# Optimization experiments

Measured on AMD Instinct MI355X. Metric: run time of the kernel, lower is better.

The kernel has to match this reference:

```python
import jax, jax.numpy as jnp
import numpy as np

THETA = 10000.0
B, S, D, H = 2, 2048, 1024, 16
DK = D // H


def setup_inputs() -> dict:
    key = jax.random.key(0)
    ks = jax.random.split(key, 5)
    std = float(np.sqrt(2.0 / (D + D)))  # get_std(in, out) with in==out==D
    x = jax.random.normal(ks[0], (B, S, D), dtype=jnp.float32)
    Wq = jax.random.normal(ks[1], (D, D), dtype=jnp.float32) * std
    Wk = jax.random.normal(ks[2], (D, D), dtype=jnp.float32) * std
    Wv = jax.random.normal(ks[3], (D, D), dtype=jnp.float32) * std
    Wo = jax.random.normal(ks[4], (D, D), dtype=jnp.float32) * std
    token_positions = jnp.broadcast_to(jnp.arange(S, dtype=jnp.int32), (B, S))
    return {"x": x, "Wq": Wq, "Wk": Wk, "Wv": Wv, "Wo": Wo,
            "token_positions": token_positions}


def _rope(x, pos):
    # x: [B, H, S, d] with interleaved pairs (even=x1, odd=x2); pos: [B, 1, S]
    d = x.shape[-1]
    inv_freq = THETA ** (-(jnp.arange(0, d, 2, dtype=jnp.float32) / d))  # [d/2]
    freqs = pos[..., None].astype(jnp.float32) * inv_freq               # [B,1,S,d/2]
    cos, sin = jnp.cos(freqs), jnp.sin(freqs)
    x1, x2 = x[..., 0::2], x[..., 1::2]
    r1 = cos * x1 - sin * x2
    r2 = sin * x1 + cos * x2
    return jnp.stack([r1, r2], axis=-1).reshape(x.shape)  # re-interleave


def reference(x, Wq, Wk, Wv, Wo, token_positions):
    # Linear is y = x @ W.T (torch weight layout [out, in])
    def split_heads(t):
        return t.reshape(B, S, H, DK).transpose(0, 2, 1, 3)  # [B,H,S,DK]

    Q = split_heads(x @ Wq.T)
    K = split_heads(x @ Wk.T)
    V = split_heads(x @ Wv.T)

    pos = token_positions[:, None, :]  # [B,1,S] broadcast over heads
    Q = _rope(Q, pos)
    K = _rope(K, pos)

    scale = 1.0 / jnp.sqrt(jnp.float32(DK))
    scores = jnp.einsum('bhqd,bhkd->bhqk', Q, K) * scale  # [B,H,S,S]
    causal = jnp.arange(S)[:, None] >= jnp.arange(S)[None, :]
    scores = jnp.where(causal, scores, -jnp.inf)
    weights = jax.nn.softmax(scores, axis=-1)
    attn = jnp.einsum('bhqk,bhkd->bhqd', weights, V)
    attn = attn.transpose(0, 2, 1, 3).reshape(B, S, D)
    return attn @ Wo.T
```

## Files before the change

kernel.cpp:

```cpp
#include <hip/hip_runtime.h>
#include <hip/hip_bf16.h>
#include <math.h>

#define B_ 2
#define S_ 2048
#define D_ 1024
#define H_ 16
#define DK_ 64

typedef __bf16 bf16_t;
typedef bf16_t bf16x8 __attribute__((ext_vector_type(8)));
typedef bf16_t bf16x4 __attribute__((ext_vector_type(4)));
typedef float f32x4 __attribute__((ext_vector_type(4)));

__device__ __forceinline__ void gload16(const void* g, void* lds_base_uniform) {
  __builtin_amdgcn_global_load_lds(
      (const __attribute__((address_space(1))) unsigned int*)g,
      (__attribute__((address_space(3))) unsigned int*)lds_base_uniform, 16, 0, 0);
}

__global__ __launch_bounds__(256) void cast_bf16_vec(const float* __restrict__ in,
                                                     bf16_t* __restrict__ out, int n4) {
  int i = blockIdx.x * 256 + threadIdx.x;
  if (i >= n4) return;
  float4 f = reinterpret_cast<const float4*>(in)[i];
  bf16x4 o;
  o[0] = (bf16_t)f.x; o[1] = (bf16_t)f.y; o[2] = (bf16_t)f.z; o[3] = (bf16_t)f.w;
  reinterpret_cast<bf16x4*>(out)[i] = o;
}

__global__ __launch_bounds__(256) void cast_weights(const float* __restrict__ Wq,
                                                    const float* __restrict__ Wk,
                                                    const float* __restrict__ Wv,
                                                    const float* __restrict__ Wo,
                                                    bf16_t* __restrict__ out) {
  int i = blockIdx.x * 256 + threadIdx.x;
  int r = i >> 18;
  const float* src = (r == 0) ? Wq : (r == 1) ? Wk : (r == 2) ? Wv : Wo;
  float4 f = reinterpret_cast<const float4*>(src)[i & 262143];
  bf16x4 o;
  o[0] = (bf16_t)f.x; o[1] = (bf16_t)f.y; o[2] = (bf16_t)f.z; o[3] = (bf16_t)f.w;
  reinterpret_cast<bf16x4*>(out)[i] = o;
}

template <bool OUT_F32>
__global__ __launch_bounds__(256) void gemm_bt(const bf16_t* __restrict__ A,
                                               const bf16_t* __restrict__ W,
                                               void* __restrict__ Cout,
                                               int Ndim, int Kdim) {
  __shared__ __attribute__((aligned(16))) bf16_t As[128][64];
  __shared__ __attribute__((aligned(16))) bf16_t Bs[128][64];
  const int bm = blockIdx.x * 128;
  const int bn = blockIdx.y * 128;
  const int tid = threadIdx.x;
  const int lane = tid & 63;
  const int w = tid >> 6;
  const int wr = w >> 1, wc = w & 1;
  const int srow_in_chunk = lane >> 3;
  const int scol = (lane & 7) << 3;

  f32x4 acc[4][4];
  for (int m = 0; m < 4; ++m)
    for (int n = 0; n < 4; ++n) acc[m][n] = (f32x4){0.f, 0.f, 0.f, 0.f};

  for (int k0 = 0; k0 < Kdim; k0 += 64) {
    __syncthreads();
#pragma unroll
    for (int it = 0; it < 4; ++it) {
      const int c = w * 4 + it;
      const int r = c * 8 + srow_in_chunk;
      gload16(&A[(size_t)(bm + r) * Kdim + k0 + scol], (char*)&As[0][0] + c * 1024);
      gload16(&W[(size_t)(bn + r) * Kdim + k0 + scol], (char*)&Bs[0][0] + c * 1024);
    }
    __syncthreads();
#pragma unroll
    for (int t = 0; t < 2; ++t) {
      const int kk = t * 32 + ((lane >> 4) << 3);
      bf16x8 af[4], bfr[4];
#pragma unroll
      for (int m = 0; m < 4; ++m)
        af[m] = *reinterpret_cast<const bf16x8*>(&As[wr * 64 + m * 16 + (lane & 15)][kk]);
#pragma unroll
      for (int n = 0; n < 4; ++n)
        bfr[n] = *reinterpret_cast<const bf16x8*>(&Bs[wc * 64 + n * 16 + (lane & 15)][kk]);
#pragma unroll
      for (int m = 0; m < 4; ++m)
#pragma unroll
        for (int n = 0; n < 4; ++n)
          acc[m][n] = __builtin_amdgcn_mfma_f32_16x16x32_bf16(af[m], bfr[n], acc[m][n], 0, 0, 0);
    }
  }

  const int rg = (lane >> 4) << 2, c0 = lane & 15;
#pragma unroll
  for (int m = 0; m < 4; ++m)
#pragma unroll
    for (int n = 0; n < 4; ++n) {
      int r = bm + wr * 64 + m * 16 + rg;
      int c = bn + wc * 64 + n * 16 + c0;
#pragma unroll
      for (int i = 0; i < 4; ++i) {
        if (OUT_F32)
          reinterpret_cast<float*>(Cout)[(size_t)(r + i) * Ndim + c] = acc[m][n][i];
        else
          reinterpret_cast<bf16_t*>(Cout)[(size_t)(r + i) * Ndim + c] = (bf16_t)acc[m][n][i];
      }
    }
}

__global__ __launch_bounds__(256) void gemm_qkv(const bf16_t* __restrict__ A,
                                                const bf16_t* __restrict__ W,
                                                const int* __restrict__ posids,
                                                bf16_t* __restrict__ Qr,
                                                bf16_t* __restrict__ Kr,
                                                bf16_t* __restrict__ Vt) {
  __shared__ __attribute__((aligned(16))) bf16_t SMEM[2][128][64];
  const int bm = blockIdx.x * 128;
  const int bn = blockIdx.y * 128;
  const int tid = threadIdx.x;
  const int lane = tid & 63;
  const int w = tid >> 6;
  const int wr = w >> 1, wc = w & 1;
  const int srow_in_chunk = lane >> 3;
  const int scol = (lane & 7) << 3;
  const int Kdim = 1024;

  f32x4 acc[4][4];
  for (int m = 0; m < 4; ++m)
    for (int n = 0; n < 4; ++n) acc[m][n] = (f32x4){0.f, 0.f, 0.f, 0.f};

  for (int k0 = 0; k0 < Kdim; k0 += 64) {
    __syncthreads();
#pragma unroll
    for (int it = 0; it < 4; ++it) {
      const int c = w * 4 + it;
      const int r = c * 8 + srow_in_chunk;
      gload16(&A[(size_t)(bm + r) * Kdim + k0 + scol], (char*)&SMEM[0][0][0] + c * 1024);
      gload16(&W[(size_t)(bn + r) * Kdim + k0 + scol], (char*)&SMEM[1][0][0] + c * 1024);
    }
    __syncthreads();
#pragma unroll
    for (int t = 0; t < 2; ++t) {
      const int kk = t * 32 + ((lane >> 4) << 3);
      bf16x8 af[4], bfr[4];
#pragma unroll
      for (int m = 0; m < 4; ++m)
        af[m] = *reinterpret_cast<const bf16x8*>(&SMEM[0][wr * 64 + m * 16 + (lane & 15)][kk]);
#pragma unroll
      for (int n = 0; n < 4; ++n)
        bfr[n] = *reinterpret_cast<const bf16x8*>(&SMEM[1][wc * 64 + n * 16 + (lane & 15)][kk]);
#pragma unroll
      for (int m = 0; m < 4; ++m)
#pragma unroll
        for (int n = 0; n < 4; ++n)
          acc[m][n] = __builtin_amdgcn_mfma_f32_16x16x32_bf16(af[m], bfr[n], acc[m][n], 0, 0, 0);
    }
  }

  const int region = bn >> 10;
  const int h0 = (bn & 1023) >> 6;
  const int b = bm >> 11;
  const int sblk = bm & 2047;
  char* Cs = (char*)&SMEM[0][0][0];
  const int rg = (lane >> 4) << 2, c0 = lane & 15;

  __syncthreads();

  if (region < 2) {
#pragma unroll
    for (int m = 0; m < 4; ++m)
#pragma unroll
      for (int n = 0; n < 4; ++n) {
        const int col = wc * 64 + n * 16 + c0;
#pragma unroll
        for (int i = 0; i < 4; ++i) {
          const int row = wr * 64 + m * 16 + rg + i;
          *(bf16_t*)(Cs + row * 256 + ((col * 2) ^ ((row & 15) << 4))) = (bf16_t)acc[m][n][i];
        }
      }
    __syncthreads();
    const int sl = tid >> 1;
    const int hh = tid & 1;
    const int s = sblk + sl;
    const int bh = b * 16 + h0 + hh;
    const int p = posids[b * 2048 + s];
    bf16_t* outp = (region == 0 ? Qr : Kr) + ((size_t)bh * 2048 + s) * 64;
    const float qscale = region == 0 ? 0.125f : 1.0f;
#pragma unroll
    for (int j = 0; j < 8; ++j) {
      const int slot = hh * 8 + j;
      bf16x8 v = *(const bf16x8*)(Cs + sl * 256 + ((slot ^ (sl & 15)) << 4));
      bf16x8 ov;
#pragma unroll
      for (int e = 0; e < 8; e += 2) {
        const int ii = j * 4 + (e >> 1);
        float sn, cs2;
        __sincosf((float)p * __expf(-(float)(2 * ii) * (9.210340371976184f / 64.0f)),
                  &sn, &cs2);
        const float x1 = (float)v[e], x2 = (float)v[e + 1];
        ov[e]     = (bf16_t)((cs2 * x1 - sn * x2) * qscale);
        ov[e + 1] = (bf16_t)((sn * x1 + cs2 * x2) * qscale);
      }
      *(bf16x8*)(&outp[j * 8]) = ov;
    }
  } else {
#pragma unroll
    for (int m = 0; m < 4; ++m)
#pragma unroll
      for (int n = 0; n < 4; ++n) {
        const int col = wc * 64 + n * 16 + c0;
        const int row0 = wr * 64 + m * 16 + rg;
        bf16x4 pk;
#pragma unroll
        for (int i = 0; i < 4; ++i) pk[i] = (bf16_t)acc[m][n][i];
        *(bf16x4*)(Cs + col * 256 + ((row0 * 2) ^ ((col & 15) << 4))) = pk;
      }
    __syncthreads();
    const int dloc = tid >> 1;
    const int sg2 = tid & 1;
    const int bh = b * 16 + h0 + (dloc >> 6);
    const int d = dloc & 63;
    bf16_t* outp = Vt + ((size_t)bh * 64 + d) * 2048 + sblk + sg2 * 64;
#pragma unroll
    for (int j = 0; j < 8; ++j) {
      bf16x8 v = *(const bf16x8*)(Cs + dloc * 256 + (((sg2 * 8 + j) ^ (dloc & 15)) << 4));
      *(bf16x8*)(&outp[j * 8]) = v;
    }
  }
}

__global__ __launch_bounds__(256) void attn_kernel(const bf16_t* __restrict__ Qr,
                                                   const bf16_t* __restrict__ Kr,
                                                   const bf16_t* __restrict__ Vt,
                                                   bf16_t* __restrict__ AO) {
  const int linear = blockIdx.x;
  const int bh = linear & 31;
  const int qt = 31 - (linear >> 5);
  const int b = bh >> 4, h = bh & 15;
  const bf16_t* Qp = Qr + (size_t)bh * S_ * 64;
  const char* Kbase = (const char*)(Kr + (size_t)bh * S_ * 64);
  const char* Vbase = (const char*)(Vt + (size_t)bh * 64 * S_);
  const int tid = threadIdx.x, lane = tid & 63, w = tid >> 6;
  const int qb = qt * 64;
  const int nt = qt + 1;

  __shared__ __attribute__((aligned(16))) bf16_t Ksm[2][64][64];
  __shared__ __attribute__((aligned(16))) bf16_t Vts[2][64][64];
  __shared__ __attribute__((aligned(16))) bf16_t Psm[4][16][64];

  const int srow = lane >> 3;
  const int sslot = lane & 7;

  bf16x8 qf[2];
  {
    int qrow = qb + w * 16 + (lane & 15);
#pragma unroll
    for (int t = 0; t < 2; ++t)
      qf[t] = *reinterpret_cast<const bf16x8*>(
          &Qp[(size_t)qrow * 64 + t * 32 + ((lane >> 4) << 3)]);
  }

  f32x4 o[4];
  for (int m = 0; m < 4; ++m) o[m] = (f32x4){0.f, 0.f, 0.f, 0.f};
  float mrow = -1e30f, lrow = 0.f;

#pragma unroll
  for (int it = 0; it < 2; ++it) {
    int c = 2 * w + it;
    int row = c * 8 + srow;
    gload16(Kbase + (size_t)row * 128 + ((sslot ^ (row & 7)) << 4),
            (char*)&Ksm[0][0][0] + c * 1024);
    gload16(Vbase + (size_t)row * (S_ * 2) + ((sslot ^ (row & 7)) << 4),
            (char*)&Vts[0][0][0] + c * 1024);
  }
  __syncthreads();

  int cur = 0;
#pragma unroll 1
  for (int kt = 0; kt < nt; ++kt) {
    if (kt + 1 < nt) {
#pragma unroll
      for (int it = 0; it < 2; ++it) {
        int c = 2 * w + it;
        int row = c * 8 + srow;
        gload16(Kbase + (size_t)(kt + 1) * 8192 + (size_t)row * 128 + ((sslot ^ (row & 7)) << 4),
                (char*)&Ksm[cur ^ 1][0][0] + c * 1024);
        gload16(Vbase + (size_t)row * (S_ * 2) + (size_t)(kt + 1) * 128 + ((sslot ^ (row & 7)) << 4),
                (char*)&Vts[cur ^ 1][0][0] + c * 1024);
      }
    }

    f32x4 sacc[4];
    for (int m = 0; m < 4; ++m) sacc[m] = (f32x4){0.f, 0.f, 0.f, 0.f};
    __builtin_amdgcn_s_setprio(1);
#pragma unroll
    for (int t = 0; t < 2; ++t) {
      const int slot0 = t * 4 + (lane >> 4);
#pragma unroll
      for (int m = 0; m < 4; ++m) {
        const int R = m * 16 + (lane & 15);
        bf16x8 kfr = *reinterpret_cast<const bf16x8*>(
            (const char*)&Ksm[cur][0][0] + R * 128 + ((slot0 ^ (R & 7)) << 4));
        sacc[m] = __builtin_amdgcn_mfma_f32_16x16x32_bf16(kfr, qf[t], sacc[m], 0, 0, 0);
      }
    }
    __builtin_amdgcn_s_setprio(0);

    const int qrow = qb + w * 16 + (lane & 15);
    const int g4 = (lane >> 4) << 2;
    if (kt * 64 + 63 > qb + w * 16) {
#pragma unroll
      for (int m = 0; m < 4; ++m) {
        const int kc0 = kt * 64 + m * 16 + g4;
#pragma unroll
        for (int r = 0; r < 4; ++r)
          if (kc0 + r > qrow) sacc[m][r] = -1e30f;
      }
    }

    float mx = sacc[0][0];
#pragma unroll
    for (int m = 0; m < 4; ++m)
#pragma unroll
      for (int r = 0; r < 4; ++r) mx = fmaxf(mx, sacc[m][r]);
    mx = fmaxf(mx, __shfl_xor(mx, 16, 64));
    mx = fmaxf(mx, __shfl_xor(mx, 32, 64));
    const float mnew = fmaxf(mrow, mx);
    const float alpha = __expf(mrow - mnew);
    mrow = mnew;

    float s = 0.f;
#pragma unroll
    for (int m = 0; m < 4; ++m)
#pragma unroll
      for (int r = 0; r < 4; ++r) {
        float p = __expf(sacc[m][r] - mnew);
        sacc[m][r] = p;
        s += p;
      }
    s += __shfl_xor(s, 16, 64);
    s += __shfl_xor(s, 32, 64);
    lrow = lrow * alpha + s;

#pragma unroll
    for (int m = 0; m < 4; ++m)
#pragma unroll
      for (int r = 0; r < 4; ++r) o[m][r] *= alpha;

    {
      const int q = lane & 15;
      char* pbase = (char*)&Psm[w][0][0] + q * 128;
      const int xm = (q & 7) << 4;
#pragma unroll
      for (int m = 0; m < 4; ++m) {
        bf16x4 pk;
#pragma unroll
        for (int r = 0; r < 4; ++r) pk[r] = (bf16_t)sacc[m][r];
        *reinterpret_cast<bf16x4*>(pbase + (((m << 5) | ((lane >> 4) << 3)) ^ xm)) = pk;
      }
    }

    __builtin_amdgcn_s_setprio(1);
#pragma unroll
    for (int t = 0; t < 2; ++t) {
      const int slot0 = t * 4 + (lane >> 4);
      bf16x8 pf = *reinterpret_cast<const bf16x8*>(
          (const char*)&Psm[w][0][0] + (lane & 15) * 128 +
          (((t << 6) | ((lane >> 4) << 4)) ^ ((lane & 7) << 4)));
#pragma unroll
      for (int m = 0; m < 4; ++m) {
        const int R = m * 16 + (lane & 15);
        bf16x8 vf = *reinterpret_cast<const bf16x8*>(
            (const char*)&Vts[cur][0][0] + R * 128 + ((slot0 ^ (R & 7)) << 4));
        o[m] = __builtin_amdgcn_mfma_f32_16x16x32_bf16(vf, pf, o[m], 0, 0, 0);
      }
    }
    __builtin_amdgcn_s_setprio(0);

    __syncthreads();
    cur ^= 1;
  }

  {
    const int q = lane & 15;
    const int g4e = (lane >> 4) << 2;
    const int srw = qb + w * 16 + q;
    const float inv = 1.0f / lrow;
#pragma unroll
    for (int m = 0; m < 4; ++m) {
      bf16x4 ov;
#pragma unroll
      for (int r = 0; r < 4; ++r) ov[r] = (bf16_t)(o[m][r] * inv);
      *reinterpret_cast<bf16x4*>(
          &AO[((size_t)(b * S_ + srw)) * 1024 + h * 64 + m * 16 + g4e]) = ov;
    }
  }
}

extern "C" void kernel_launch(void* const* d_in, const int* in_sizes, int n_in,
                              void* d_out, int out_size, void* d_ws, size_t ws_size,
                              hipStream_t stream) {
  const float* x  = (const float*)d_in[0];
  const float* Wq = (const float*)d_in[1];
  const float* Wk = (const float*)d_in[2];
  const float* Wv = (const float*)d_in[3];
  const float* Wo = (const float*)d_in[4];
  const int* tp   = (const int*)d_in[5];

  char* ws = (char*)d_ws;
  bf16_t* xb   = (bf16_t*)(ws);
  bf16_t* Wcat = (bf16_t*)(ws + 8388608);
  bf16_t* Wob  = (bf16_t*)(ws + 14680064);
  bf16_t* Qr   = (bf16_t*)(ws + 41943040);
  bf16_t* Kr   = (bf16_t*)(ws + 50331648);
  bf16_t* Vt   = (bf16_t*)(ws + 58720256);
  bf16_t* AO   = (bf16_t*)(ws + 67108864);

  cast_bf16_vec<<<dim3(4096), dim3(256), 0, stream>>>(x, xb, 1048576);
  cast_weights<<<dim3(4096), dim3(256), 0, stream>>>(Wq, Wk, Wv, Wo, Wcat);

  gemm_qkv<<<dim3(32, 24), dim3(256), 0, stream>>>(xb, Wcat, tp, Qr, Kr, Vt);
  attn_kernel<<<dim3(1024), dim3(256), 0, stream>>>(Qr, Kr, Vt, AO);
  gemm_bt<true><<<dim3(32, 8), dim3(256), 0, stream>>>(AO, Wob, d_out, 1024, 1024);

  (void)in_sizes; (void)n_in; (void)out_size; (void)ws_size;
}
```

Before: 133.7 us.

## Double attention query tile to 128 rows with 8 waves per block

```diff
diff --git a/kernel.cpp b/kernel.cpp
--- a/kernel.cpp
+++ b/kernel.cpp
@@ -229,31 +229,32 @@
   }
 }
 
-__global__ __launch_bounds__(256) void attn_kernel(const bf16_t* __restrict__ Qr,
+__global__ __launch_bounds__(512) void attn_kernel(const bf16_t* __restrict__ Qr,
                                                    const bf16_t* __restrict__ Kr,
                                                    const bf16_t* __restrict__ Vt,
                                                    bf16_t* __restrict__ AO) {
   const int linear = blockIdx.x;
   const int bh = linear & 31;
-  const int qt = 31 - (linear >> 5);
+  const int qt = 15 - (linear >> 5);
   const int b = bh >> 4, h = bh & 15;
   const bf16_t* Qp = Qr + (size_t)bh * S_ * 64;
   const char* Kbase = (const char*)(Kr + (size_t)bh * S_ * 64);
   const char* Vbase = (const char*)(Vt + (size_t)bh * 64 * S_);
   const int tid = threadIdx.x, lane = tid & 63, w = tid >> 6;
-  const int qb = qt * 64;
-  const int nt = qt + 1;
+  const int qb = qt * 128;
+  const int nt = 2 * qt + 2;
+  const int wr0 = qb + w * 16;
 
   __shared__ __attribute__((aligned(16))) bf16_t Ksm[2][64][64];
   __shared__ __attribute__((aligned(16))) bf16_t Vts[2][64][64];
-  __shared__ __attribute__((aligned(16))) bf16_t Psm[4][16][64];
+  __shared__ __attribute__((aligned(16))) bf16_t Psm[8][16][64];
 
   const int srow = lane >> 3;
   const int sslot = lane & 7;
 
   bf16x8 qf[2];
   {
-    int qrow = qb + w * 16 + (lane & 15);
+    int qrow = wr0 + (lane & 15);
 #pragma unroll
     for (int t = 0; t < 2; ++t)
       qf[t] = *reinterpret_cast<const bf16x8*>(
@@ -264,14 +265,12 @@
   for (int m = 0; m < 4; ++m) o[m] = (f32x4){0.f, 0.f, 0.f, 0.f};
   float mrow = -1e30f, lrow = 0.f;
 
-#pragma unroll
-  for (int it = 0; it < 2; ++it) {
-    int c = 2 * w + it;
-    int row = c * 8 + srow;
+  {
+    int row = w * 8 + srow;
     gload16(Kbase + (size_t)row * 128 + ((sslot ^ (row & 7)) << 4),
-            (char*)&Ksm[0][0][0] + c * 1024);
+            (char*)&Ksm[0][0][0] + w * 1024);
     gload16(Vbase + (size_t)row * (S_ * 2) + ((sslot ^ (row & 7)) << 4),
-            (char*)&Vts[0][0][0] + c * 1024);
+            (char*)&Vts[0][0][0] + w * 1024);
   }
   __syncthreads();
 
@@ -279,103 +278,101 @@
 #pragma unroll 1
   for (int kt = 0; kt < nt; ++kt) {
     if (kt + 1 < nt) {
-#pragma unroll
-      for (int it = 0; it < 2; ++it) {
-        int c = 2 * w + it;
-        int row = c * 8 + srow;
-        gload16(Kbase + (size_t)(kt + 1) * 8192 + (size_t)row * 128 + ((sslot ^ (row & 7)) << 4),
-                (char*)&Ksm[cur ^ 1][0][0] + c * 1024);
-        gload16(Vbase + (size_t)row * (S_ * 2) + (size_t)(kt + 1) * 128 + ((sslot ^ (row & 7)) << 4),
-                (char*)&Vts[cur ^ 1][0][0] + c * 1024);
-      }
-    }
-
-    f32x4 sacc[4];
-    for (int m = 0; m < 4; ++m) sacc[m] = (f32x4){0.f, 0.f, 0.f, 0.f};
-    __builtin_amdgcn_s_setprio(1);
-#pragma unroll
-    for (int t = 0; t < 2; ++t) {
-      const int slot0 = t * 4 + (lane >> 4);
-#pragma unroll
-      for (int m = 0; m < 4; ++m) {
-        const int R = m * 16 + (lane & 15);
-        bf16x8 kfr = *reinterpret_cast<const bf16x8*>(
-            (const char*)&Ksm[cur][0][0] + R * 128 + ((slot0 ^ (R & 7)) << 4));
-        sacc[m] = __builtin_amdgcn_mfma_f32_16x16x32_bf16(kfr, qf[t], sacc[m], 0, 0, 0);
-      }
-    }
-    __builtin_amdgcn_s_setprio(0);
-
-    const int qrow = qb + w * 16 + (lane & 15);
-    const int g4 = (lane >> 4) << 2;
-    if (kt * 64 + 63 > qb + w * 16) {
-#pragma unroll
-      for (int m = 0; m < 4; ++m) {
-        const int kc0 = kt * 64 + m * 16 + g4;
-#pragma unroll
-        for (int r = 0; r < 4; ++r)
-          if (kc0 + r > qrow) sacc[m][r] = -1e30f;
-      }
-    }
-
-    float mx = sacc[0][0];
-#pragma unroll
-    for (int m = 0; m < 4; ++m)
-#pragma unroll
-      for (int r = 0; r < 4; ++r) mx = fmaxf(mx, sacc[m][r]);
-    mx = fmaxf(mx, __shfl_xor(mx, 16, 64));
-    mx = fmaxf(mx, __shfl_xor(mx, 32, 64));
-    const float mnew = fmaxf(mrow, mx);
-    const float alpha = __expf(mrow - mnew);
-    mrow = mnew;
-
-    float s = 0.f;
-#pragma unroll
-    for (int m = 0; m < 4; ++m)
-#pragma unroll
-      for (int r = 0; r < 4; ++r) {
-        float p = __expf(sacc[m][r] - mnew);
-        sacc[m][r] = p;
-        s += p;
-      }
-    s += __shfl_xor(s, 16, 64);
-    s += __shfl_xor(s, 32, 64);
-    lrow = lrow * alpha + s;
-
-#pragma unroll
-    for (int m = 0; m < 4; ++m)
-#pragma unroll
-      for (int r = 0; r < 4; ++r) o[m][r] *= alpha;
-
-    {
-      const int q = lane & 15;
-      char* pbase = (char*)&Psm[w][0][0] + q * 128;
-      const int xm = (q & 7) << 4;
-#pragma unroll
-      for (int m = 0; m < 4; ++m) {
-        bf16x4 pk;
-#pragma unroll
-        for (int r = 0; r < 4; ++r) pk[r] = (bf16_t)sacc[m][r];
-        *reinterpret_cast<bf16x4*>(pbase + (((m << 5) | ((lane >> 4) << 3)) ^ xm)) = pk;
-      }
-    }
-
-    __builtin_amdgcn_s_setprio(1);
-#pragma unroll
-    for (int t = 0; t < 2; ++t) {
-      const int slot0 = t * 4 + (lane >> 4);
-      bf16x8 pf = *reinterpret_cast<const bf16x8*>(
-          (const char*)&Psm[w][0][0] + (lane & 15) * 128 +
-          (((t << 6) | ((lane >> 4) << 4)) ^ ((lane & 7) << 4)));
-#pragma unroll
-      for (int m = 0; m < 4; ++m) {
-        const int R = m * 16 + (lane & 15);
-        bf16x8 vf = *reinterpret_cast<const bf16x8*>(
-            (const char*)&Vts[cur][0][0] + R * 128 + ((slot0 ^ (R & 7)) << 4));
-        o[m] = __builtin_amdgcn_mfma_f32_16x16x32_bf16(vf, pf, o[m], 0, 0, 0);
-      }
-    }
-    __builtin_amdgcn_s_setprio(0);
+      int row = w * 8 + srow;
+      gload16(Kbase + (size_t)(kt + 1) * 8192 + (size_t)row * 128 + ((sslot ^ (row & 7)) << 4),
+              (char*)&Ksm[cur ^ 1][0][0] + w * 1024);
+      gload16(Vbase + (size_t)row * (S_ * 2) + (size_t)(kt + 1) * 128 + ((sslot ^ (row & 7)) << 4),
+              (char*)&Vts[cur ^ 1][0][0] + w * 1024);
+    }
+
+    if (kt * 64 <= wr0 + 15) {
+      f32x4 sacc[4];
+      for (int m = 0; m < 4; ++m) sacc[m] = (f32x4){0.f, 0.f, 0.f, 0.f};
+      __builtin_amdgcn_s_setprio(1);
+#pragma unroll
+      for (int t = 0; t < 2; ++t) {
+        const int slot0 = t * 4 + (lane >> 4);
+#pragma unroll
+        for (int m = 0; m < 4; ++m) {
+          const int R = m * 16 + (lane & 15);
+          bf16x8 kfr = *reinterpret_cast<const bf16x8*>(
+              (const char*)&Ksm[cur][0][0] + R * 128 + ((slot0 ^ (R & 7)) << 4));
+          sacc[m] = __builtin_amdgcn_mfma_f32_16x16x32_bf16(kfr, qf[t], sacc[m], 0, 0, 0);
+        }
+      }
+      __builtin_amdgcn_s_setprio(0);
+
+      const int qrow = wr0 + (lane & 15);
+      const int g4 = (lane >> 4) << 2;
+      if (kt * 64 + 63 > wr0) {
+#pragma unroll
+        for (int m = 0; m < 4; ++m) {
+          const int kc0 = kt * 64 + m * 16 + g4;
+#pragma unroll
+          for (int r = 0; r < 4; ++r)
+            if (kc0 + r > qrow) sacc[m][r] = -1e30f;
+        }
+      }
+
+      float mx = sacc[0][0];
+#pragma unroll
+      for (int m = 0; m < 4; ++m)
+#pragma unroll
+        for (int r = 0; r < 4; ++r) mx = fmaxf(mx, sacc[m][r]);
+      mx = fmaxf(mx, __shfl_xor(mx, 16, 64));
+      mx = fmaxf(mx, __shfl_xor(mx, 32, 64));
+      const float mnew = fmaxf(mrow, mx);
+      const float alpha = __expf(mrow - mnew);
+      mrow = mnew;
+
+      float s = 0.f;
+#pragma unroll
+      for (int m = 0; m < 4; ++m)
+#pragma unroll
+        for (int r = 0; r < 4; ++r) {
+          float p = __expf(sacc[m][r] - mnew);
+          sacc[m][r] = p;
+          s += p;
+        }
+      s += __shfl_xor(s, 16, 64);
+      s += __shfl_xor(s, 32, 64);
+      lrow = lrow * alpha + s;
+
+#pragma unroll
+      for (int m = 0; m < 4; ++m)
+#pragma unroll
+        for (int r = 0; r < 4; ++r) o[m][r] *= alpha;
+
+      {
+        const int q = lane & 15;
+        char* pbase = (char*)&Psm[w][0][0] + q * 128;
+        const int xm = (q & 7) << 4;
+#pragma unroll
+        for (int m = 0; m < 4; ++m) {
+          bf16x4 pk;
+#pragma unroll
+          for (int r = 0; r < 4; ++r) pk[r] = (bf16_t)sacc[m][r];
+          *reinterpret_cast<bf16x4*>(pbase + (((m << 5) | ((lane >> 4) << 3)) ^ xm)) = pk;
+        }
+      }
+
+      __builtin_amdgcn_s_setprio(1);
+#pragma unroll
+      for (int t = 0; t < 2; ++t) {
+        const int slot0 = t * 4 + (lane >> 4);
+        bf16x8 pf = *reinterpret_cast<const bf16x8*>(
+            (const char*)&Psm[w][0][0] + (lane & 15) * 128 +
+            (((t << 6) | ((lane >> 4) << 4)) ^ ((lane & 7) << 4)));
+#pragma unroll
+        for (int m = 0; m < 4; ++m) {
+          const int R = m * 16 + (lane & 15);
+          bf16x8 vf = *reinterpret_cast<const bf16x8*>(
+              (const char*)&Vts[cur][0][0] + R * 128 + ((slot0 ^ (R & 7)) << 4));
+          o[m] = __builtin_amdgcn_mfma_f32_16x16x32_bf16(vf, pf, o[m], 0, 0, 0);
+        }
+      }
+      __builtin_amdgcn_s_setprio(0);
+    }
 
     __syncthreads();
     cur ^= 1;
@@ -384,7 +381,7 @@
   {
     const int q = lane & 15;
     const int g4e = (lane >> 4) << 2;
-    const int srw = qb + w * 16 + q;
+    const int srw = wr0 + q;
     const float inv = 1.0f / lrow;
 #pragma unroll
     for (int m = 0; m < 4; ++m) {
@@ -420,7 +417,7 @@
   cast_weights<<<dim3(4096), dim3(256), 0, stream>>>(Wq, Wk, Wv, Wo, Wcat);
 
   gemm_qkv<<<dim3(32, 24), dim3(256), 0, stream>>>(xb, Wcat, tp, Qr, Kr, Vt);
-  attn_kernel<<<dim3(1024), dim3(256), 0, stream>>>(Qr, Kr, Vt, AO);
+  attn_kernel<<<dim3(512), dim3(512), 0, stream>>>(Qr, Kr, Vt, AO);
   gemm_bt<true><<<dim3(32, 8), dim3(256), 0, stream>>>(AO, Wob, d_out, 1024, 1024);
 
   (void)in_sizes; (void)n_in; (void)out_size; (void)ws_size;
```

Result: no change. 136.1 us (+1.8%).

## Use 8-wave GEMM blocks with XOR-swizzled LDS tiles for QKV and output projections

Applied to the files above, without the earlier changes.

```diff
diff --git a/kernel.cpp b/kernel.cpp
--- a/kernel.cpp
+++ b/kernel.cpp
@@ -44,7 +44,7 @@
 }
 
 template <bool OUT_F32>
-__global__ __launch_bounds__(256) void gemm_bt(const bf16_t* __restrict__ A,
+__global__ __launch_bounds__(512) void gemm_bt(const bf16_t* __restrict__ A,
                                                const bf16_t* __restrict__ W,
                                                void* __restrict__ Cout,
                                                int Ndim, int Kdim) {
@@ -55,38 +55,45 @@
   const int tid = threadIdx.x;
   const int lane = tid & 63;
   const int w = tid >> 6;
-  const int wr = w >> 1, wc = w & 1;
-  const int srow_in_chunk = lane >> 3;
-  const int scol = (lane & 7) << 3;
-
-  f32x4 acc[4][4];
+  const int wm = w >> 2, wn = w & 3;
+  const int srow_c = lane >> 3;
+  const int sslot = lane & 7;
+
+  f32x4 acc[4][2];
   for (int m = 0; m < 4; ++m)
-    for (int n = 0; n < 4; ++n) acc[m][n] = (f32x4){0.f, 0.f, 0.f, 0.f};
+    for (int n = 0; n < 2; ++n) acc[m][n] = (f32x4){0.f, 0.f, 0.f, 0.f};
 
   for (int k0 = 0; k0 < Kdim; k0 += 64) {
     __syncthreads();
 #pragma unroll
-    for (int it = 0; it < 4; ++it) {
-      const int c = w * 4 + it;
-      const int r = c * 8 + srow_in_chunk;
-      gload16(&A[(size_t)(bm + r) * Kdim + k0 + scol], (char*)&As[0][0] + c * 1024);
-      gload16(&W[(size_t)(bn + r) * Kdim + k0 + scol], (char*)&Bs[0][0] + c * 1024);
+    for (int it = 0; it < 2; ++it) {
+      const int c = 2 * w + it;
+      const int row = c * 8 + srow_c;
+      const int col = ((sslot ^ (row & 7)) << 3);
+      gload16(&A[(size_t)(bm + row) * Kdim + k0 + col], (char*)&As[0][0] + c * 1024);
+      gload16(&W[(size_t)(bn + row) * Kdim + k0 + col], (char*)&Bs[0][0] + c * 1024);
     }
     __syncthreads();
 #pragma unroll
     for (int t = 0; t < 2; ++t) {
-      const int kk = t * 32 + ((lane >> 4) << 3);
-      bf16x8 af[4], bfr[4];
+      const int slot0 = t * 4 + (lane >> 4);
+      bf16x8 af[4], bfr[2];
+#pragma unroll
+      for (int m = 0; m < 4; ++m) {
+        const int R = wm * 64 + m * 16 + (lane & 15);
+        af[m] = *reinterpret_cast<const bf16x8*>(
+            (const char*)&As[0][0] + R * 128 + ((slot0 ^ (R & 7)) << 4));
+      }
+#pragma unroll
+      for (int n = 0; n < 2; ++n) {
+        const int R = wn * 32 + n * 16 + (lane & 15);
+        bfr[n] = *reinterpret_cast<const bf16x8*>(
+            (const char*)&Bs[0][0] + R * 128 + ((slot0 ^ (R & 7)) << 4));
+      }
 #pragma unroll
       for (int m = 0; m < 4; ++m)
-        af[m] = *reinterpret_cast<const bf16x8*>(&As[wr * 64 + m * 16 + (lane & 15)][kk]);
-#pragma unroll
-      for (int n = 0; n < 4; ++n)
-        bfr[n] = *reinterpret_cast<const bf16x8*>(&Bs[wc * 64 + n * 16 + (lane & 15)][kk]);
-#pragma unroll
-      for (int m = 0; m < 4; ++m)
-#pragma unroll
-        for (int n = 0; n < 4; ++n)
+#pragma unroll
+        for (int n = 0; n < 2; ++n)
           acc[m][n] = __builtin_amdgcn_mfma_f32_16x16x32_bf16(af[m], bfr[n], acc[m][n], 0, 0, 0);
     }
   }
@@ -95,9 +102,9 @@
 #pragma unroll
   for (int m = 0; m < 4; ++m)
 #pragma unroll
-    for (int n = 0; n < 4; ++n) {
-      int r = bm + wr * 64 + m * 16 + rg;
-      int c = bn + wc * 64 + n * 16 + c0;
+    for (int n = 0; n < 2; ++n) {
+      int r = bm + wm * 64 + m * 16 + rg;
+      int c = bn + wn * 32 + n * 16 + c0;
 #pragma unroll
       for (int i = 0; i < 4; ++i) {
         if (OUT_F32)
@@ -108,7 +115,7 @@
     }
 }
 
-__global__ __launch_bounds__(256) void gemm_qkv(const bf16_t* __restrict__ A,
+__global__ __launch_bounds__(512) void gemm_qkv(const bf16_t* __restrict__ A,
                                                 const bf16_t* __restrict__ W,
                                                 const int* __restrict__ posids,
                                                 bf16_t* __restrict__ Qr,
@@ -120,39 +127,46 @@
   const int tid = threadIdx.x;
   const int lane = tid & 63;
   const int w = tid >> 6;
-  const int wr = w >> 1, wc = w & 1;
-  const int srow_in_chunk = lane >> 3;
-  const int scol = (lane & 7) << 3;
+  const int wm = w >> 2, wn = w & 3;
+  const int srow_c = lane >> 3;
+  const int sslot = lane & 7;
   const int Kdim = 1024;
 
-  f32x4 acc[4][4];
+  f32x4 acc[4][2];
   for (int m = 0; m < 4; ++m)
-    for (int n = 0; n < 4; ++n) acc[m][n] = (f32x4){0.f, 0.f, 0.f, 0.f};
+    for (int n = 0; n < 2; ++n) acc[m][n] = (f32x4){0.f, 0.f, 0.f, 0.f};
 
   for (int k0 = 0; k0 < Kdim; k0 += 64) {
     __syncthreads();
 #pragma unroll
-    for (int it = 0; it < 4; ++it) {
-      const int c = w * 4 + it;
-      const int r = c * 8 + srow_in_chunk;
-      gload16(&A[(size_t)(bm + r) * Kdim + k0 + scol], (char*)&SMEM[0][0][0] + c * 1024);
-      gload16(&W[(size_t)(bn + r) * Kdim + k0 + scol], (char*)&SMEM[1][0][0] + c * 1024);
+    for (int it = 0; it < 2; ++it) {
+      const int c = 2 * w + it;
+      const int row = c * 8 + srow_c;
+      const int col = ((sslot ^ (row & 7)) << 3);
+      gload16(&A[(size_t)(bm + row) * Kdim + k0 + col], (char*)&SMEM[0][0][0] + c * 1024);
+      gload16(&W[(size_t)(bn + row) * Kdim + k0 + col], (char*)&SMEM[1][0][0] + c * 1024);
     }
     __syncthreads();
 #pragma unroll
     for (int t = 0; t < 2; ++t) {
-      const int kk = t * 32 + ((lane >> 4) << 3);
-      bf16x8 af[4], bfr[4];
+      const int slot0 = t * 4 + (lane >> 4);
+      bf16x8 af[4], bfr[2];
+#pragma unroll
+      for (int m = 0; m < 4; ++m) {
+        const int R = wm * 64 + m * 16 + (lane & 15);
+        af[m] = *reinterpret_cast<const bf16x8*>(
+            (const char*)&SMEM[0][0][0] + R * 128 + ((slot0 ^ (R & 7)) << 4));
+      }
+#pragma unroll
+      for (int n = 0; n < 2; ++n) {
+        const int R = wn * 32 + n * 16 + (lane & 15);
+        bfr[n] = *reinterpret_cast<const bf16x8*>(
+            (const char*)&SMEM[1][0][0] + R * 128 + ((slot0 ^ (R & 7)) << 4));
+      }
 #pragma unroll
       for (int m = 0; m < 4; ++m)
-        af[m] = *reinterpret_cast<const bf16x8*>(&SMEM[0][wr * 64 + m * 16 + (lane & 15)][kk]);
-#pragma unroll
-      for (int n = 0; n < 4; ++n)
-        bfr[n] = *reinterpret_cast<const bf16x8*>(&SMEM[1][wc * 64 + n * 16 + (lane & 15)][kk]);
-#pragma unroll
-      for (int m = 0; m < 4; ++m)
-#pragma unroll
-        for (int n = 0; n < 4; ++n)
+#pragma unroll
+        for (int n = 0; n < 2; ++n)
           acc[m][n] = __builtin_amdgcn_mfma_f32_16x16x32_bf16(af[m], bfr[n], acc[m][n], 0, 0, 0);
     }
   }
@@ -170,24 +184,26 @@
 #pragma unroll
     for (int m = 0; m < 4; ++m)
 #pragma unroll
-      for (int n = 0; n < 4; ++n) {
-        const int col = wc * 64 + n * 16 + c0;
+      for (int n = 0; n < 2; ++n) {
+        const int col = wn * 32 + n * 16 + c0;
 #pragma unroll
         for (int i = 0; i < 4; ++i) {
-          const int row = wr * 64 + m * 16 + rg + i;
+          const int row = wm * 64 + m * 16 + rg + i;
           *(bf16_t*)(Cs + row * 256 + ((col * 2) ^ ((row & 15) << 4))) = (bf16_t)acc[m][n][i];
         }
       }
     __syncthreads();
-    const int sl = tid >> 1;
-    const int hh = tid & 1;
+    const int sl = tid >> 2;
+    const int hh = (tid >> 1) & 1;
+    const int jh = tid & 1;
     const int s = sblk + sl;
     const int bh = b * 16 + h0 + hh;
     const int p = posids[b * 2048 + s];
     bf16_t* outp = (region == 0 ? Qr : Kr) + ((size_t)bh * 2048 + s) * 64;
     const float qscale = region == 0 ? 0.125f : 1.0f;
 #pragma unroll
-    for (int j = 0; j < 8; ++j) {
+    for (int jj = 0; jj < 4; ++jj) {
+      const int j = jh * 4 + jj;
       const int slot = hh * 8 + j;
       bf16x8 v = *(const bf16x8*)(Cs + sl * 256 + ((slot ^ (sl & 15)) << 4));
       bf16x8 ov;
@@ -207,22 +223,24 @@
 #pragma unroll
     for (int m = 0; m < 4; ++m)
 #pragma unroll
-      for (int n = 0; n < 4; ++n) {
-        const int col = wc * 64 + n * 16 + c0;
-        const int row0 = wr * 64 + m * 16 + rg;
+      for (int n = 0; n < 2; ++n) {
+        const int col = wn * 32 + n * 16 + c0;
+        const int row0 = wm * 64 + m * 16 + rg;
         bf16x4 pk;
 #pragma unroll
         for (int i = 0; i < 4; ++i) pk[i] = (bf16_t)acc[m][n][i];
         *(bf16x4*)(Cs + col * 256 + ((row0 * 2) ^ ((col & 15) << 4))) = pk;
       }
     __syncthreads();
-    const int dloc = tid >> 1;
-    const int sg2 = tid & 1;
+    const int dloc = tid >> 2;
+    const int sg2 = (tid >> 1) & 1;
+    const int jh = tid & 1;
     const int bh = b * 16 + h0 + (dloc >> 6);
     const int d = dloc & 63;
     bf16_t* outp = Vt + ((size_t)bh * 64 + d) * 2048 + sblk + sg2 * 64;
 #pragma unroll
-    for (int j = 0; j < 8; ++j) {
+    for (int jj = 0; jj < 4; ++jj) {
+      const int j = jh * 4 + jj;
       bf16x8 v = *(const bf16x8*)(Cs + dloc * 256 + (((sg2 * 8 + j) ^ (dloc & 15)) << 4));
       *(bf16x8*)(&outp[j * 8]) = v;
     }
@@ -419,9 +437,9 @@
   cast_bf16_vec<<<dim3(4096), dim3(256), 0, stream>>>(x, xb, 1048576);
   cast_weights<<<dim3(4096), dim3(256), 0, stream>>>(Wq, Wk, Wv, Wo, Wcat);
 
-  gemm_qkv<<<dim3(32, 24), dim3(256), 0, stream>>>(xb, Wcat, tp, Qr, Kr, Vt);
+  gemm_qkv<<<dim3(32, 24), dim3(512), 0, stream>>>(xb, Wcat, tp, Qr, Kr, Vt);
   attn_kernel<<<dim3(1024), dim3(256), 0, stream>>>(Qr, Kr, Vt, AO);
-  gemm_bt<true><<<dim3(32, 8), dim3(256), 0, stream>>>(AO, Wob, d_out, 1024, 1024);
+  gemm_bt<true><<<dim3(32, 8), dim3(512), 0, stream>>>(AO, Wob, d_out, 1024, 1024);
 
   (void)in_sizes; (void)n_in; (void)out_size; (void)ws_size;
 }
```

Result: faster. 118.0 us (-11.7%).
